# Optimization experiments

Measured on AMD Instinct MI355X. Metric: run time of the kernel, lower is better.

Reference implementation:

```python
import jax, jax.numpy as jnp
import numpy as np

B, C, T, H, W = 8, 64, 32, 56, 56
WIN = 7
EPS = 1e-5


def setup_inputs() -> dict:
    key = jax.random.key(0)
    k1, k2, k3, k4 = jax.random.split(key, 4)
    x = jax.random.normal(k1, (B, C, T, H, W), dtype=jnp.float32)
    # BatchNorm3d affine params (randomized slightly around init for nontrivial math)
    gamma = 1.0 + 0.1 * jax.random.normal(k2, (C,), dtype=jnp.float32)
    beta = 0.1 * jax.random.normal(k3, (C,), dtype=jnp.float32)
    # rpconv1d weight [2] ~ init [1,0] plus noise so both taps contribute
    rpw = jnp.array([1.0, 0.0], dtype=jnp.float32) + 0.1 * jax.random.normal(k4, (2,), dtype=jnp.float32)
    return {"x": x, "gamma": gamma, "beta": beta, "rpw": rpw, "w": WIN}


def reference(x, gamma, beta, rpw, w):
    # x: [B, C, T, H, W]
    Bs, Cs, Ts, Hs, Ws = x.shape
    # rank-pooling weights: for window position k (0-based), 2*(k+1) - w - 1
    coeff = (2.0 * jnp.arange(1, w + 1, dtype=x.dtype) - w - 1)
    # causal padding with w-1 zero frames at the front of T
    xp = jnp.pad(x, ((0, 0), (0, 0), (w - 1, 0), (0, 0), (0, 0)))
    rp = jnp.zeros_like(x)
    for k in range(w):  # small fixed window, fuses under XLA
        rp = rp + coeff[k] * jax.lax.dynamic_slice_in_dim(xp, k, Ts, axis=2)
    # BatchNorm3d (training-mode batch stats over B,T,H,W per channel) + ReLU
    mean = jnp.mean(rp, axis=(0, 2, 3, 4), keepdims=True)
    var = jnp.var(rp, axis=(0, 2, 3, 4), keepdims=True)
    bn = (rp - mean) * jax.lax.rsqrt(var + EPS)
    bn = bn * gamma.reshape(1, -1, 1, 1, 1) + beta.reshape(1, -1, 1, 1, 1)
    y = jax.nn.relu(bn)
    # gating: (y + 1) * x
    g = (y + 1.0) * x
    # rpconv1d(2->1, kernel 1, no bias): out = rpw[0]*x + rpw[1]*g
    return rpw[0] * x + rpw[1] * g
```

## Files before the change

kernel.cpp:

```cpp
#include <hip/hip_runtime.h>

#define B_      8
#define C_      64
#define T_      32
#define HW_     3136
#define HW4_    784
#define NPC_    802816.0
#define EPS_    1e-5
#define CHUNKS_ 7
#define BLK_    128

typedef float f32x4 __attribute__((ext_vector_type(4)));

__device__ __forceinline__ float rp_tap(float a0, float a1, float a2,
                                        float a4, float a5, float a6) {
    return 6.f * (a0 - a6) + 4.f * (a1 - a5) + 2.f * (a2 - a4);
}

__global__ __launch_bounds__(BLK_, 4) void datt_pass1(
    const float* __restrict__ x, double2* __restrict__ part)
{
    const int bc    = blockIdx.y;
    const int chunk = blockIdx.x;
    const int hw4   = chunk * BLK_ + threadIdx.x;

    float s = 0.f, q = 0.f;
    if (hw4 < HW4_) {
        const float4* xp = (const float4*)(x + (size_t)bc * (T_ * HW_)) + hw4;
        float4 win[7];
#pragma unroll
        for (int k = 0; k < 7; ++k) win[k] = make_float4(0.f, 0.f, 0.f, 0.f);
#pragma unroll
        for (int t = 0; t < T_; ++t) {
            float4 xv = xp[(size_t)t * HW4_];
            win[t % 7] = xv;
            const float4 a1 = win[(t + 6) % 7];
            const float4 a2 = win[(t + 5) % 7];
            const float4 a4 = win[(t + 3) % 7];
            const float4 a5 = win[(t + 2) % 7];
            const float4 a6 = win[(t + 1) % 7];
            float rx = rp_tap(xv.x, a1.x, a2.x, a4.x, a5.x, a6.x);
            float ry = rp_tap(xv.y, a1.y, a2.y, a4.y, a5.y, a6.y);
            float rz = rp_tap(xv.z, a1.z, a2.z, a4.z, a5.z, a6.z);
            float rw = rp_tap(xv.w, a1.w, a2.w, a4.w, a5.w, a6.w);
            s += rx + ry + rz + rw;
            q += rx * rx + ry * ry + rz * rz + rw * rw;
        }
    }
#pragma unroll
    for (int off = 32; off; off >>= 1) {
        s += __shfl_down(s, off);
        q += __shfl_down(q, off);
    }
    __shared__ float ls[2], lq[2];
    const int wid  = threadIdx.x >> 6;
    const int lane = threadIdx.x & 63;
    if (lane == 0) { ls[wid] = s; lq[wid] = q; }
    __syncthreads();
    if (threadIdx.x == 0) {
        const int tile = bc * CHUNKS_ + chunk;
        part[tile] = make_double2((double)(ls[0] + ls[1]),
                                  (double)(lq[0] + lq[1]));
    }
}

__global__ __launch_bounds__(BLK_, 4) void datt_pass2(
    const float* __restrict__ x,
    const double2* __restrict__ part,
    const float* __restrict__ gamma,
    const float* __restrict__ beta,
    const float* __restrict__ rpw,
    float* __restrict__ out)
{
    const int bc    = blockIdx.y;
    const int c     = bc & (C_ - 1);
    const int chunk = blockIdx.x;
    const int tid   = threadIdx.x;

    __shared__ float lss[2];

    if (tid < 64) {
        double s = 0.0, q = 0.0;
        if (tid < B_ * CHUNKS_) {
            const int b  = tid / CHUNKS_;
            const int ch = tid - b * CHUNKS_;
            double2 p = part[(b * C_ + c) * CHUNKS_ + ch];
            s = p.x; q = p.y;
        }
#pragma unroll
        for (int off = 32; off; off >>= 1) {
            s += __shfl_down(s, off);
            q += __shfl_down(q, off);
        }
        if (tid == 0) {
            double mean = s / NPC_;
            double var  = q / NPC_ - mean * mean;
            float rstd  = (float)(1.0 / sqrt(var + EPS_));
            float sc    = gamma[c] * rstd;
            lss[0] = sc;
            lss[1] = beta[c] - (float)mean * sc;
        }
    }
    __syncthreads();

    const int hw4 = chunk * BLK_ + tid;
    if (hw4 >= HW4_) return;

    const float sc = lss[0];
    const float sh = lss[1];
    const float r1 = rpw[1];
    const float A  = rpw[0] + r1;

    const f32x4* xp = (const f32x4*)(x   + (size_t)bc * (T_ * HW_)) + hw4;
    f32x4*       op = (f32x4*)      (out + (size_t)bc * (T_ * HW_)) + hw4;

    f32x4 win[7];
#pragma unroll
    for (int k = 0; k < 7; ++k) win[k] = (f32x4)(0.f);
#pragma unroll
    for (int t = 0; t < T_; ++t) {
        f32x4 xv = xp[(size_t)t * HW4_];
        win[t % 7] = xv;
        const f32x4 a1 = win[(t + 6) % 7];
        const f32x4 a2 = win[(t + 5) % 7];
        const f32x4 a4 = win[(t + 3) % 7];
        const f32x4 a5 = win[(t + 2) % 7];
        const f32x4 a6 = win[(t + 1) % 7];
        f32x4 o;
#pragma unroll
        for (int j = 0; j < 4; ++j) {
            float yj = fmaxf(fmaf(rp_tap(xv[j], a1[j], a2[j], a4[j], a5[j], a6[j]),
                                  sc, sh), 0.f);
            o[j] = xv[j] * fmaf(r1, yj, A);
        }
        __builtin_nontemporal_store(o, &op[(size_t)t * HW4_]);
    }
}

extern "C" void kernel_launch(void* const* d_in, const int* in_sizes, int n_in,
                              void* d_out, int out_size, void* d_ws, size_t ws_size,
                              hipStream_t stream) {
    const float* x     = (const float*)d_in[0];
    const float* gamma = (const float*)d_in[1];
    const float* beta  = (const float*)d_in[2];
    const float* rpw   = (const float*)d_in[3];
    float* out = (float*)d_out;

    double2* part = (double2*)d_ws;

    dim3 grid(CHUNKS_, B_ * C_);
    datt_pass1<<<grid, BLK_, 0, stream>>>(x, part);
    datt_pass2<<<grid, BLK_, 0, stream>>>(x, part, gamma, beta, rpw, out);
}
```

Before: 380.7 us.

## Use one 512-thread block per (b,c) plane with two float4 columns per thread

Replaces the 7-chunk x 512 grid of 128-thread blocks with 512 blocks of 512 threads. Each block covers a whole (b,c) plane and each thread handles up to two float4 columns, which removes the partial-tile padding waste and reduces the per-channel partials from 56 to 8. The cost is double the register sliding windows per thread and only 512 blocks in total, which lowers occupancy and may hide memory latency less well on a 256-CU part.

```diff
diff --git a/kernel.cpp b/kernel.cpp
--- a/kernel.cpp
+++ b/kernel.cpp
@@ -5,10 +5,11 @@
 #define T_      32
 #define HW_     3136
 #define HW4_    784
+#define PLANE_  (T_ * HW_)
 #define NPC_    802816.0
 #define EPS_    1e-5
-#define CHUNKS_ 7
-#define BLK_    128
+#define BLK_    512
+#define TAIL_   (HW4_ - BLK_)
 
 typedef float f32x4 __attribute__((ext_vector_type(4)));
 
@@ -17,54 +18,64 @@
     return 6.f * (a0 - a6) + 4.f * (a1 - a5) + 2.f * (a2 - a4);
 }
 
-__global__ __launch_bounds__(BLK_, 4) void datt_pass1(
+__device__ __forceinline__ float rp_tap4_sq(const f32x4& a0, const f32x4& a1,
+                                            const f32x4& a2, const f32x4& a4,
+                                            const f32x4& a5, const f32x4& a6,
+                                            float& s, float& q) {
+#pragma unroll
+    for (int j = 0; j < 4; ++j) {
+        float r = rp_tap(a0[j], a1[j], a2[j], a4[j], a5[j], a6[j]);
+        s += r;
+        q += r * r;
+    }
+    return 0.f;
+}
+
+__global__ __launch_bounds__(BLK_, 2) void datt_pass1(
     const float* __restrict__ x, double2* __restrict__ part)
 {
-    const int bc    = blockIdx.y;
-    const int chunk = blockIdx.x;
-    const int hw4   = chunk * BLK_ + threadIdx.x;
+    const int bc  = blockIdx.x;
+    const int tid = threadIdx.x;
+    const bool act1 = tid < TAIL_;
+
+    const f32x4* xp = (const f32x4*)(x + (size_t)bc * PLANE_);
+
+    f32x4 w0[7], w1[7];
+#pragma unroll
+    for (int k = 0; k < 7; ++k) { w0[k] = (f32x4)(0.f); w1[k] = (f32x4)(0.f); }
 
     float s = 0.f, q = 0.f;
-    if (hw4 < HW4_) {
-        const float4* xp = (const float4*)(x + (size_t)bc * (T_ * HW_)) + hw4;
-        float4 win[7];
 #pragma unroll
-        for (int k = 0; k < 7; ++k) win[k] = make_float4(0.f, 0.f, 0.f, 0.f);
-#pragma unroll
-        for (int t = 0; t < T_; ++t) {
-            float4 xv = xp[(size_t)t * HW4_];
-            win[t % 7] = xv;
-            const float4 a1 = win[(t + 6) % 7];
-            const float4 a2 = win[(t + 5) % 7];
-            const float4 a4 = win[(t + 3) % 7];
-            const float4 a5 = win[(t + 2) % 7];
-            const float4 a6 = win[(t + 1) % 7];
-            float rx = rp_tap(xv.x, a1.x, a2.x, a4.x, a5.x, a6.x);
-            float ry = rp_tap(xv.y, a1.y, a2.y, a4.y, a5.y, a6.y);
-            float rz = rp_tap(xv.z, a1.z, a2.z, a4.z, a5.z, a6.z);
-            float rw = rp_tap(xv.w, a1.w, a2.w, a4.w, a5.w, a6.w);
-            s += rx + ry + rz + rw;
-            q += rx * rx + ry * ry + rz * rz + rw * rw;
-        }
+    for (int t = 0; t < T_; ++t) {
+        const int row = t * HW4_;
+        f32x4 x0 = xp[row + tid];
+        f32x4 x1 = act1 ? xp[row + BLK_ + tid] : (f32x4)(0.f);
+        w0[t % 7] = x0;
+        w1[t % 7] = x1;
+        rp_tap4_sq(x0, w0[(t + 6) % 7], w0[(t + 5) % 7],
+                       w0[(t + 3) % 7], w0[(t + 2) % 7], w0[(t + 1) % 7], s, q);
+        rp_tap4_sq(x1, w1[(t + 6) % 7], w1[(t + 5) % 7],
+                       w1[(t + 3) % 7], w1[(t + 2) % 7], w1[(t + 1) % 7], s, q);
     }
 #pragma unroll
     for (int off = 32; off; off >>= 1) {
         s += __shfl_down(s, off);
         q += __shfl_down(q, off);
     }
-    __shared__ float ls[2], lq[2];
-    const int wid  = threadIdx.x >> 6;
-    const int lane = threadIdx.x & 63;
-    if (lane == 0) { ls[wid] = s; lq[wid] = q; }
+    __shared__ double ls[8], lq[8];
+    const int wid  = tid >> 6;
+    const int lane = tid & 63;
+    if (lane == 0) { ls[wid] = (double)s; lq[wid] = (double)q; }
     __syncthreads();
-    if (threadIdx.x == 0) {
-        const int tile = bc * CHUNKS_ + chunk;
-        part[tile] = make_double2((double)(ls[0] + ls[1]),
-                                  (double)(lq[0] + lq[1]));
+    if (tid == 0) {
+        double S = 0.0, Q = 0.0;
+#pragma unroll
+        for (int i = 0; i < 8; ++i) { S += ls[i]; Q += lq[i]; }
+        part[bc] = make_double2(S, Q);
     }
 }
 
-__global__ __launch_bounds__(BLK_, 4) void datt_pass2(
+__global__ __launch_bounds__(BLK_, 2) void datt_pass2(
     const float* __restrict__ x,
     const double2* __restrict__ part,
     const float* __restrict__ gamma,
@@ -72,23 +83,21 @@
     const float* __restrict__ rpw,
     float* __restrict__ out)
 {
-    const int bc    = blockIdx.y;
-    const int c     = bc & (C_ - 1);
-    const int chunk = blockIdx.x;
-    const int tid   = threadIdx.x;
+    const int bc  = blockIdx.x;
+    const int c   = bc & (C_ - 1);
+    const int tid = threadIdx.x;
+    const bool act1 = tid < TAIL_;
 
     __shared__ float lss[2];
 
     if (tid < 64) {
         double s = 0.0, q = 0.0;
-        if (tid < B_ * CHUNKS_) {
-            const int b  = tid / CHUNKS_;
-            const int ch = tid - b * CHUNKS_;
-            double2 p = part[(b * C_ + c) * CHUNKS_ + ch];
+        if (tid < B_) {
+            double2 p = part[tid * C_ + c];
             s = p.x; q = p.y;
         }
 #pragma unroll
-        for (int off = 32; off; off >>= 1) {
+        for (int off = 4; off; off >>= 1) {
             s += __shfl_down(s, off);
             q += __shfl_down(q, off);
         }
@@ -103,37 +112,52 @@
     }
     __syncthreads();
 
-    const int hw4 = chunk * BLK_ + tid;
-    if (hw4 >= HW4_) return;
-
     const float sc = lss[0];
     const float sh = lss[1];
     const float r1 = rpw[1];
     const float A  = rpw[0] + r1;
 
-    const f32x4* xp = (const f32x4*)(x   + (size_t)bc * (T_ * HW_)) + hw4;
-    f32x4*       op = (f32x4*)      (out + (size_t)bc * (T_ * HW_)) + hw4;
+    const f32x4* xp = (const f32x4*)(x   + (size_t)bc * PLANE_);
+    f32x4*       op = (f32x4*)      (out + (size_t)bc * PLANE_);
 
-    f32x4 win[7];
+    f32x4 w0[7], w1[7];
 #pragma unroll
-    for (int k = 0; k < 7; ++k) win[k] = (f32x4)(0.f);
+    for (int k = 0; k < 7; ++k) { w0[k] = (f32x4)(0.f); w1[k] = (f32x4)(0.f); }
+
 #pragma unroll
     for (int t = 0; t < T_; ++t) {
-        f32x4 xv = xp[(size_t)t * HW4_];
-        win[t % 7] = xv;
-        const f32x4 a1 = win[(t + 6) % 7];
-        const f32x4 a2 = win[(t + 5) % 7];
-        const f32x4 a4 = win[(t + 3) % 7];
-        const f32x4 a5 = win[(t + 2) % 7];
-        const f32x4 a6 = win[(t + 1) % 7];
-        f32x4 o;
+        const int row = t * HW4_;
+        f32x4 x0 = xp[row + tid];
+        f32x4 x1 = act1 ? xp[row + BLK_ + tid] : (f32x4)(0.f);
+        w0[t % 7] = x0;
+        w1[t % 7] = x1;
+
+        f32x4 o0, o1;
+        {
+            const f32x4 a1 = w0[(t + 6) % 7], a2 = w0[(t + 5) % 7];
+            const f32x4 a4 = w0[(t + 3) % 7], a5 = w0[(t + 2) % 7];
+            const f32x4 a6 = w0[(t + 1) % 7];
 #pragma unroll
-        for (int j = 0; j < 4; ++j) {
-            float yj = fmaxf(fmaf(rp_tap(xv[j], a1[j], a2[j], a4[j], a5[j], a6[j]),
-                                  sc, sh), 0.f);
-            o[j] = xv[j] * fmaf(r1, yj, A);
+            for (int j = 0; j < 4; ++j) {
+                float yj = fmaxf(fmaf(rp_tap(x0[j], a1[j], a2[j], a4[j], a5[j], a6[j]),
+                                      sc, sh), 0.f);
+                o0[j] = x0[j] * fmaf(r1, yj, A);
+            }
         }
-        __builtin_nontemporal_store(o, &op[(size_t)t * HW4_]);
+        {
+            const f32x4 a1 = w1[(t + 6) % 7], a2 = w1[(t + 5) % 7];
+            const f32x4 a4 = w1[(t + 3) % 7], a5 = w1[(t + 2) % 7];
+            const f32x4 a6 = w1[(t + 1) % 7];
+#pragma unroll
+            for (int j = 0; j < 4; ++j) {
+                float yj = fmaxf(fmaf(rp_tap(x1[j], a1[j], a2[j], a4[j], a5[j], a6[j]),
+                                      sc, sh), 0.f);
+                o1[j] = x1[j] * fmaf(r1, yj, A);
+            }
+        }
+        __builtin_nontemporal_store(o0, &op[row + tid]);
+        if (act1)
+            __builtin_nontemporal_store(o1, &op[row + BLK_ + tid]);
     }
 }
 
@@ -148,7 +172,6 @@
 
     double2* part = (double2*)d_ws;
 
-    dim3 grid(CHUNKS_, B_ * C_);
-    datt_pass1<<<grid, BLK_, 0, stream>>>(x, part);
-    datt_pass2<<<grid, BLK_, 0, stream>>>(x, part, gamma, beta, rpw, out);
+    datt_pass1<<<dim3(B_ * C_), BLK_, 0, stream>>>(x, part);
+    datt_pass2<<<dim3(B_ * C_), BLK_, 0, stream>>>(x, part, gamma, beta, rpw, out);
 }
```

After: 384.0 us. About the same (+0.8%).
